# Optimization experiments

Hardware: AMD Instinct MI355X
Metric: run time of the kernel (lower is better)

The kernel has to match this reference:

```python
import jax, jax.numpy as jnp
import numpy as np

N_NODES = 50000
N_EDGES = 800000
IN_DIM = 128
IN_CH = 64
HIDDEN = 64
OUT_CH = 128
NUM_CLS = 16
NUM_GRAPHS = 512


def setup_inputs() -> dict:
    key = jax.random.key(0)
    ks = jax.random.split(key, 16)
    s = 0.02
    x = jax.random.normal(ks[0], (N_NODES, IN_DIM), jnp.float32)
    edge_index = jax.random.randint(ks[1], (2, N_EDGES), 0, N_NODES, jnp.int64)
    batch = jnp.sort(jax.random.randint(ks[2], (N_NODES,), 0, NUM_GRAPHS, jnp.int64))
    return {
        "x": x,
        "edge_index": edge_index,
        "batch": batch,
        "num_graphs": NUM_GRAPHS,
        "w_stage1": jax.random.normal(ks[3], (IN_DIM, IN_CH), jnp.float32) * s,
        "b_stage1": jnp.zeros((IN_CH,), jnp.float32),
        "rel1_w": jax.random.normal(ks[4], (IN_CH, HIDDEN), jnp.float32) * s,
        "rel1_b": jnp.zeros((HIDDEN,), jnp.float32),
        "root1_w": jax.random.normal(ks[5], (IN_CH, HIDDEN), jnp.float32) * s,
        "rel2_w": jax.random.normal(ks[6], (HIDDEN, 2 * HIDDEN), jnp.float32) * s,
        "rel2_b": jnp.zeros((2 * HIDDEN,), jnp.float32),
        "root2_w": jax.random.normal(ks[7], (HIDDEN, 2 * HIDDEN), jnp.float32) * s,
        "rel3_w": jax.random.normal(ks[8], (2 * HIDDEN, OUT_CH), jnp.float32) * s,
        "rel3_b": jnp.zeros((OUT_CH,), jnp.float32),
        "root3_w": jax.random.normal(ks[9], (2 * HIDDEN, OUT_CH), jnp.float32) * s,
        "lin_w": jax.random.normal(ks[10], (OUT_CH, NUM_CLS), jnp.float32) * s,
        "lin_b": jnp.zeros((NUM_CLS,), jnp.float32),
    }


def graph_conv(x, src, dst, rel_w, rel_b, root_w, n_nodes):
    # PyG GraphConv(aggr='add'): lin_rel(sum_{j in N(i)} x_j) + lin_root(x_i)
    agg = jax.ops.segment_sum(x[src], dst, num_segments=n_nodes)  # [N, in]
    return agg @ rel_w + rel_b + x @ root_w


def reference(x, edge_index, batch, num_graphs,
              w_stage1, b_stage1,
              rel1_w, rel1_b, root1_w,
              rel2_w, rel2_b, root2_w,
              rel3_w, rel3_b, root3_w,
              lin_w, lin_b):
    src, dst = edge_index[0], edge_index[1]
    n = x.shape[0]
    h = x @ w_stage1 + b_stage1                                   # [N, IN_CH]
    h = jax.nn.relu(graph_conv(h, src, dst, rel1_w, rel1_b, root1_w, n))
    h = jax.nn.relu(graph_conv(h, src, dst, rel2_w, rel2_b, root2_w, n))
    h = jax.nn.relu(graph_conv(h, src, dst, rel3_w, rel3_b, root3_w, n))
    # global mean pool over graphs
    sums = jax.ops.segment_sum(h, batch, num_segments=num_graphs)  # [G, OUT_CH]
    cnt = jax.ops.segment_sum(jnp.ones((n,), h.dtype), batch, num_segments=num_graphs)
    pooled = sums / jnp.maximum(cnt, 1.0)[:, None]
    # dropout treated as identity (deterministic eval reference)
    return pooled @ lin_w + lin_b                                  # [G, NUM_CLS]
```

## Files before the change

kernel.cpp:

```cpp
#include <hip/hip_runtime.h>
#include <hip/hip_bf16.h>

#define N_NODES 50000
#define N_EDGES 800000
#define IN_DIM  128
#define IN_CH   64
#define HIDDEN  64
#define OUT_CH  128
#define NUM_CLS 16
#define NUM_G   512
#define NBUK    ((N_NODES + 255) >> 8)
#define BCAP    6144
#define EPB_A   4096
#define S1BLK   782

typedef __attribute__((ext_vector_type(8))) short short8;
typedef __attribute__((ext_vector_type(4))) float f32x4;

__device__ inline float bits2f(unsigned short u) {
  unsigned x = (unsigned)u << 16;
  float f;
  __builtin_memcpy(&f, &x, 4);
  return f;
}
__device__ inline unsigned short f2bits(float v) {
  __hip_bfloat16 b = __float2bfloat16(v);
  unsigned short s;
  __builtin_memcpy(&s, &b, 2);
  return s;
}
__device__ inline short8 zero8() {
  short8 z;
#pragma unroll
  for (int i = 0; i < 8; ++i) z[i] = 0;
  return z;
}
__device__ inline void acc2(float& a0, float& a1, unsigned v) {
  a0 += bits2f((unsigned short)v);
  a1 += bits2f((unsigned short)(v >> 16));
}
__device__ inline void accu4(float* a, uint4 v) {
  acc2(a[0], a[1], v.x); acc2(a[2], a[3], v.y);
  acc2(a[4], a[5], v.z); acc2(a[6], a[7], v.w);
}

__device__ inline void stage1_wave(const float* __restrict__ Ap,
    const short* __restrict__ Wa, const float* __restrict__ bias,
    unsigned short* __restrict__ outp, int rbase, int lane) {
  constexpr int DIN = 128, DOUT = 64, KT = DIN / 32, CT = DOUT / 16;
  const int m = lane & 15;
  const int q = lane >> 4;
  const int row = rbase + m;
  const bool ok = row < N_NODES;

  short8 afr[KT];
#pragma unroll
  for (int kt = 0; kt < KT; ++kt) {
    short8 f = zero8();
    if (ok) {
      const float* ap = Ap + (size_t)row * DIN + kt * 32 + q * 8;
      float4 x0 = *(const float4*)ap;
      float4 x1 = *(const float4*)(ap + 4);
      f[0] = (short)f2bits(x0.x); f[1] = (short)f2bits(x0.y);
      f[2] = (short)f2bits(x0.z); f[3] = (short)f2bits(x0.w);
      f[4] = (short)f2bits(x1.x); f[5] = (short)f2bits(x1.y);
      f[6] = (short)f2bits(x1.z); f[7] = (short)f2bits(x1.w);
    }
    afr[kt] = f;
  }
#pragma unroll
  for (int ct = 0; ct < CT; ++ct) {
    f32x4 c = {0.f, 0.f, 0.f, 0.f};
#pragma unroll
    for (int kt = 0; kt < KT; ++kt) {
      short8 b = *(const short8*)(Wa + ((size_t)(kt * CT + ct) * 64 + lane) * 8);
      c = __builtin_amdgcn_mfma_f32_16x16x32_bf16(afr[kt], b, c, 0, 0, 0);
    }
    float bv = bias[ct * 16 + m];
#pragma unroll
    for (int r = 0; r < 4; ++r) {
      int ro = rbase + q * 4 + r;
      if (ro < N_NODES) outp[(size_t)ro * DOUT + ct * 16 + m] = f2bits(c[r] + bv);
    }
  }
}

template <int DIN, int DOUT>
__global__ __launch_bounds__(64) void k_fused(
    const unsigned short* __restrict__ h, const int* __restrict__ esrc,
    const int* __restrict__ off, const short* __restrict__ Wa,
    const short* __restrict__ Wh, const float* __restrict__ bias,
    unsigned short* __restrict__ outp) {
  constexpr int KT = DIN / 32;
  constexpr int CT = DOUT / 16;
  const int lane = threadIdx.x;
  const int m = lane & 15;
  const int q = lane >> 4;
  const int node = blockIdx.x * 16 + m;

  float acc[KT][8];
#pragma unroll
  for (int kt = 0; kt < KT; ++kt)
#pragma unroll
    for (int j = 0; j < 8; ++j) acc[kt][j] = 0.f;

  {
    int e = off[node], end = off[node + 1];
    const unsigned short* hq = h + q * 8;
    for (; e + 2 <= end; e += 2) {
      int s0 = esrc[e], s1 = esrc[e + 1];
      const unsigned short* r0 = hq + (size_t)s0 * DIN;
      const unsigned short* r1 = hq + (size_t)s1 * DIN;
#pragma unroll
      for (int kt = 0; kt < KT; ++kt) {
        uint4 va = *(const uint4*)(r0 + kt * 32);
        uint4 vb = *(const uint4*)(r1 + kt * 32);
        accu4(acc[kt], va);
        accu4(acc[kt], vb);
      }
    }
    if (e < end) {
      const unsigned short* r0 = hq + (size_t)esrc[e] * DIN;
#pragma unroll
      for (int kt = 0; kt < KT; ++kt)
        accu4(acc[kt], *(const uint4*)(r0 + kt * 32));
    }
  }

  short8 afr[KT], hfr[KT];
#pragma unroll
  for (int kt = 0; kt < KT; ++kt) {
    short8 f;
#pragma unroll
    for (int j = 0; j < 8; ++j) f[j] = (short)f2bits(acc[kt][j]);
    afr[kt] = f;
    hfr[kt] = *(const short8*)(h + (size_t)node * DIN + kt * 32 + q * 8);
  }

  const int rbase = blockIdx.x * 16;
#pragma unroll
  for (int ct = 0; ct < CT; ++ct) {
    f32x4 c = {0.f, 0.f, 0.f, 0.f};
#pragma unroll
    for (int kt = 0; kt < KT; ++kt) {
      short8 b = *(const short8*)(Wa + ((size_t)(kt * CT + ct) * 64 + lane) * 8);
      c = __builtin_amdgcn_mfma_f32_16x16x32_bf16(afr[kt], b, c, 0, 0, 0);
      short8 bh = *(const short8*)(Wh + ((size_t)(kt * CT + ct) * 64 + lane) * 8);
      c = __builtin_amdgcn_mfma_f32_16x16x32_bf16(hfr[kt], bh, c, 0, 0, 0);
    }
    float bv = bias[ct * 16 + m];
#pragma unroll
    for (int r = 0; r < 4; ++r) {
      int row = rbase + q * 4 + r;
      outp[(size_t)row * DOUT + ct * 16 + m] = f2bits(fmaxf(c[r] + bv, 0.f));
    }
  }
}

template <int DIN, int DOUT>
__device__ inline void pack1(const float* __restrict__ W, short* __restrict__ o,
                             int t) {
  constexpr int CT = DOUT / 16;
  int j = t & 7;
  int lane = (t >> 3) & 63;
  int kc = t >> 9;
  int ct = kc % CT;
  int kt = kc / CT;
  int k = kt * 32 + (lane >> 4) * 8 + j;
  int n = ct * 16 + (lane & 15);
  o[t] = (short)f2bits(W[k * DOUT + n]);
}

struct PackArgs {
  const float *w1, *r1, *o1, *r2, *o2, *r3, *o3;
  short *w1p, *r1p, *o1p, *r2p, *o2p, *r3p, *o3p;
};

__device__ inline void packflat(const PackArgs& a, int t) {
  if      (t < 8192)  pack1<128, 64>(a.w1, a.w1p, t);
  else if (t < 12288) pack1<64, 64>(a.r1, a.r1p, t - 8192);
  else if (t < 16384) pack1<64, 64>(a.o1, a.o1p, t - 12288);
  else if (t < 24576) pack1<64, 128>(a.r2, a.r2p, t - 16384);
  else if (t < 32768) pack1<64, 128>(a.o2, a.o2p, t - 24576);
  else if (t < 49152) pack1<128, 128>(a.r3, a.r3p, t - 32768);
  else if (t < 65536) pack1<128, 128>(a.o3, a.o3p, t - 49152);
}

__global__ __launch_bounds__(256) void k_bucketA(const int* __restrict__ src,
    const int* __restrict__ dst, int* __restrict__ bcnt,
    unsigned* __restrict__ bbuf, PackArgs pk) {
  __shared__ int hist[NBUK], sbase[NBUK], lcur[NBUK];
  const int t = threadIdx.x;

  {
    int g0 = blockIdx.x * 256 + t;
    packflat(pk, g0);
    packflat(pk, g0 + 50176);
  }

  for (int i = t; i < NBUK; i += 256) { hist[i] = 0; lcur[i] = 0; }
  __syncthreads();
  const int e0 = blockIdx.x * EPB_A;
  int s_[16], d_[16];
  int cnt = 0;
#pragma unroll
  for (int k = 0; k < 16; ++k) {
    int e = e0 + k * 256 + t;
    if (e < N_EDGES) {
      s_[cnt] = src[e]; d_[cnt] = dst[e];
      atomicAdd(&hist[d_[cnt] >> 8], 1);
      cnt++;
    }
  }
  __syncthreads();
  for (int i = t; i < NBUK; i += 256) sbase[i] = atomicAdd(&bcnt[i], hist[i]);
  __syncthreads();
  for (int k = 0; k < cnt; ++k) {
    int b = d_[k] >> 8;
    int pos = sbase[b] + atomicAdd(&lcur[b], 1);
    if (pos < BCAP)
      bbuf[(size_t)b * BCAP + pos] =
          ((unsigned)s_[k] << 8) | ((unsigned)d_[k] & 255u);
  }
}

__global__ __launch_bounds__(256) void k_bfin_s1(const int* __restrict__ bcnt,
    const unsigned* __restrict__ bbuf, int* __restrict__ off,
    int* __restrict__ esrc,
    const float* __restrict__ x, const short* __restrict__ w1p,
    const float* __restrict__ b1, unsigned short* __restrict__ P) {
  if (blockIdx.x >= NBUK) {
    const int bs = blockIdx.x - NBUK;
    const int wave = threadIdx.x >> 6;
    const int lane = threadIdx.x & 63;
    stage1_wave(x, w1p, b1, P, bs * 64 + wave * 16, lane);
    return;
  }

  __shared__ int cnt[256], s[256], soff[256];
  const int b = blockIdx.x;
  const int t = threadIdx.x;

  int bv0 = (t < NBUK) ? min(bcnt[t], BCAP) : 0;
  s[t] = bv0;
  __syncthreads();
  for (int st = 1; st < 256; st <<= 1) {
    int v = (t >= st) ? s[t - st] : 0;
    __syncthreads();
    s[t] += v;
    __syncthreads();
  }
  __shared__ int bbase_s;
  if (t == b) bbase_s = s[t] - bv0;
  if (b == 0 && t == NBUK - 1) off[N_NODES] = s[t];
  __syncthreads();
  const int bb = bbase_s;

  cnt[t] = 0;
  __syncthreads();
  int n = min(bcnt[b], BCAP);
  for (int i = t; i < n; i += 256)
    atomicAdd(&cnt[bbuf[(size_t)b * BCAP + i] & 255u], 1);
  __syncthreads();
  int v0 = cnt[t];
  s[t] = v0;
  __syncthreads();
  for (int st = 1; st < 256; st <<= 1) {
    int v = (t >= st) ? s[t - st] : 0;
    __syncthreads();
    s[t] += v;
    __syncthreads();
  }
  int myoff = bb + s[t] - v0;
  int node = b * 256 + t;
  if (node < N_NODES) off[node] = myoff;
  soff[t] = myoff;
  cnt[t] = 0;
  __syncthreads();
  for (int i = t; i < n; i += 256) {
    unsigned p = bbuf[(size_t)b * BCAP + i];
    int l = (int)(p & 255u);
    int r = atomicAdd(&cnt[l], 1);
    esrc[soff[l] + r] = (int)(p >> 8);
  }
}

__device__ inline int lbound(const int* __restrict__ a, int n, int v) {
  int lo = 0, hi = n;
  while (lo < hi) {
    int m = (lo + hi) >> 1;
    if (a[m] < v) lo = m + 1; else hi = m;
  }
  return lo;
}

__global__ __launch_bounds__(128) void k_poolhead(const unsigned short* __restrict__ h3,
    const int* __restrict__ batch, const float* __restrict__ lw,
    const float* __restrict__ lb, float* __restrict__ out) {
  __shared__ float sp[128];
  int g = blockIdx.x;
  int t = threadIdx.x;
  int lo = lbound(batch, N_NODES, g);
  int hi = lbound(batch, N_NODES, g + 1);
  float a0 = 0.f, a1 = 0.f, a2 = 0.f, a3 = 0.f;
  int r = lo;
  for (; r + 4 <= hi; r += 4) {
    a0 += bits2f(h3[(size_t)(r + 0) * OUT_CH + t]);
    a1 += bits2f(h3[(size_t)(r + 1) * OUT_CH + t]);
    a2 += bits2f(h3[(size_t)(r + 2) * OUT_CH + t]);
    a3 += bits2f(h3[(size_t)(r + 3) * OUT_CH + t]);
  }
  for (; r < hi; ++r) a0 += bits2f(h3[(size_t)r * OUT_CH + t]);
  float inv = (hi > lo) ? 1.f / (float)(hi - lo) : 0.f;
  sp[t] = ((a0 + a1) + (a2 + a3)) * inv;
  __syncthreads();
  if (t < NUM_CLS) {
    float s = lb[t];
#pragma unroll
    for (int k = 0; k < OUT_CH; ++k) s = fmaf(sp[k], lw[k * NUM_CLS + t], s);
    out[g * NUM_CLS + t] = s;
  }
}

extern "C" void kernel_launch(void* const* d_in, const int* in_sizes, int n_in,
                              void* d_out, int out_size, void* d_ws, size_t ws_size,
                              hipStream_t stream) {
  const float* x      = (const float*)d_in[0];
  const int*   ei     = (const int*)d_in[1];
  const int*   batch  = (const int*)d_in[2];
  const float* w1     = (const float*)d_in[4];
  const float* b1     = (const float*)d_in[5];
  const float* rel1w  = (const float*)d_in[6];
  const float* rel1b  = (const float*)d_in[7];
  const float* root1w = (const float*)d_in[8];
  const float* rel2w  = (const float*)d_in[9];
  const float* rel2b  = (const float*)d_in[10];
  const float* root2w = (const float*)d_in[11];
  const float* rel3w  = (const float*)d_in[12];
  const float* rel3b  = (const float*)d_in[13];
  const float* root3w = (const float*)d_in[14];
  const float* linw   = (const float*)d_in[15];
  const float* linb   = (const float*)d_in[16];
  const int* src = ei;
  const int* dst = ei + N_EDGES;
  float* out = (float*)d_out;

  unsigned short* P = (unsigned short*)d_ws;
  unsigned short* Q = P + (size_t)N_NODES * 128;
  unsigned short* R = Q + (size_t)N_NODES * 128;
  short* WP = (short*)(R + (size_t)N_NODES * 128);
  short* w1p  = WP;
  short* r1p  = w1p + 8192;
  short* o1p  = r1p + 4096;
  short* r2p  = o1p + 4096;
  short* o2p  = r2p + 8192;
  short* r3p  = o2p + 8192;
  short* o3p  = r3p + 16384;
  int* off     = (int*)(o3p + 16384);
  int* bcnt    = off + (N_NODES + 1);
  int* esrc    = bcnt + NBUK + 3;
  unsigned* bbuf = (unsigned*)(esrc + N_EDGES);

  PackArgs pk = {w1, rel1w, root1w, rel2w, root2w, rel3w, root3w,
                 w1p, r1p, o1p, r2p, o2p, r3p, o3p};

  hipMemsetAsync(bcnt, 0, NBUK * sizeof(int), stream);
  k_bucketA<<<(N_EDGES + EPB_A - 1) / EPB_A, 256, 0, stream>>>(src, dst, bcnt,
                                                               bbuf, pk);
  k_bfin_s1<<<NBUK + S1BLK, 256, 0, stream>>>(bcnt, bbuf, off, esrc,
                                              x, w1p, b1, P);

  const int GF = (N_NODES + 15) / 16;

  k_fused<64, 64><<<GF, 64, 0, stream>>>(P, esrc, off, r1p, o1p, rel1b, R);
  k_fused<64, 128><<<GF, 64, 0, stream>>>(R, esrc, off, r2p, o2p, rel2b, Q);
  k_fused<128, 128><<<GF, 64, 0, stream>>>(Q, esrc, off, r3p, o3p, rel3b, P);
  k_poolhead<<<NUM_G, 128, 0, stream>>>(P, batch, linw, linb, out);
}
```

Measured before the change: 240.4 us.

## Split fused GraphConv feature dimension across two waves with LDS reduction

Each 16-node block now uses two wavefronts, each gathering and accumulating half of the input feature dimension (K split). Each wave computes partial MFMA products for half the output tiles, exchanges them through shared memory, and sums them before bias and ReLU. This doubles wave-level parallelism for the edge gather, giving more memory-level parallelism and latency hiding. The cost is a block barrier, LDS traffic for the partial sums, and each wave re-reading the edge indices.

After: 244.6 us. Within noise of the previous version (+1.8%).

```diff
diff --git a/kernel.cpp b/kernel.cpp
--- a/kernel.cpp
+++ b/kernel.cpp
@@ -86,33 +86,37 @@
 }
 
 template <int DIN, int DOUT>
-__global__ __launch_bounds__(64) void k_fused(
+__global__ __launch_bounds__(128) void k_fused(
     const unsigned short* __restrict__ h, const int* __restrict__ esrc,
     const int* __restrict__ off, const short* __restrict__ Wa,
     const short* __restrict__ Wh, const float* __restrict__ bias,
     unsigned short* __restrict__ outp) {
   constexpr int KT = DIN / 32;
   constexpr int CT = DOUT / 16;
-  const int lane = threadIdx.x;
+  constexpr int KTH = KT / 2;
+  constexpr int CTH = CT / 2;
+  __shared__ float comb[CT * 4 * 64];
+  const int wid = threadIdx.x >> 6;
+  const int lane = threadIdx.x & 63;
   const int m = lane & 15;
   const int q = lane >> 4;
   const int node = blockIdx.x * 16 + m;
 
-  float acc[KT][8];
-#pragma unroll
-  for (int kt = 0; kt < KT; ++kt)
+  float acc[KTH][8];
+#pragma unroll
+  for (int kt = 0; kt < KTH; ++kt)
 #pragma unroll
     for (int j = 0; j < 8; ++j) acc[kt][j] = 0.f;
 
   {
     int e = off[node], end = off[node + 1];
-    const unsigned short* hq = h + q * 8;
+    const unsigned short* hq = h + q * 8 + wid * (KTH * 32);
     for (; e + 2 <= end; e += 2) {
       int s0 = esrc[e], s1 = esrc[e + 1];
       const unsigned short* r0 = hq + (size_t)s0 * DIN;
       const unsigned short* r1 = hq + (size_t)s1 * DIN;
 #pragma unroll
-      for (int kt = 0; kt < KT; ++kt) {
+      for (int kt = 0; kt < KTH; ++kt) {
         uint4 va = *(const uint4*)(r0 + kt * 32);
         uint4 vb = *(const uint4*)(r1 + kt * 32);
         accu4(acc[kt], va);
@@ -122,37 +126,57 @@
     if (e < end) {
       const unsigned short* r0 = hq + (size_t)esrc[e] * DIN;
 #pragma unroll
-      for (int kt = 0; kt < KT; ++kt)
+      for (int kt = 0; kt < KTH; ++kt)
         accu4(acc[kt], *(const uint4*)(r0 + kt * 32));
     }
   }
 
-  short8 afr[KT], hfr[KT];
-#pragma unroll
-  for (int kt = 0; kt < KT; ++kt) {
+  short8 afr[KTH], hfr[KTH];
+#pragma unroll
+  for (int kt = 0; kt < KTH; ++kt) {
     short8 f;
 #pragma unroll
     for (int j = 0; j < 8; ++j) f[j] = (short)f2bits(acc[kt][j]);
     afr[kt] = f;
-    hfr[kt] = *(const short8*)(h + (size_t)node * DIN + kt * 32 + q * 8);
+    hfr[kt] = *(const short8*)(h + (size_t)node * DIN +
+                               (wid * KTH + kt) * 32 + q * 8);
   }
 
   const int rbase = blockIdx.x * 16;
 #pragma unroll
-  for (int ct = 0; ct < CT; ++ct) {
+  for (int i = 0; i < CTH; ++i) {
+    const int ct = (1 - wid) * CTH + i;
     f32x4 c = {0.f, 0.f, 0.f, 0.f};
 #pragma unroll
-    for (int kt = 0; kt < KT; ++kt) {
-      short8 b = *(const short8*)(Wa + ((size_t)(kt * CT + ct) * 64 + lane) * 8);
+    for (int kt = 0; kt < KTH; ++kt) {
+      const int gkt = wid * KTH + kt;
+      short8 b = *(const short8*)(Wa + ((size_t)(gkt * CT + ct) * 64 + lane) * 8);
       c = __builtin_amdgcn_mfma_f32_16x16x32_bf16(afr[kt], b, c, 0, 0, 0);
-      short8 bh = *(const short8*)(Wh + ((size_t)(kt * CT + ct) * 64 + lane) * 8);
+      short8 bh = *(const short8*)(Wh + ((size_t)(gkt * CT + ct) * 64 + lane) * 8);
+      c = __builtin_amdgcn_mfma_f32_16x16x32_bf16(hfr[kt], bh, c, 0, 0, 0);
+    }
+#pragma unroll
+    for (int r = 0; r < 4; ++r) comb[(ct * 4 + r) * 64 + lane] = c[r];
+  }
+  __syncthreads();
+#pragma unroll
+  for (int i = 0; i < CTH; ++i) {
+    const int ct = wid * CTH + i;
+    f32x4 c = {0.f, 0.f, 0.f, 0.f};
+#pragma unroll
+    for (int kt = 0; kt < KTH; ++kt) {
+      const int gkt = wid * KTH + kt;
+      short8 b = *(const short8*)(Wa + ((size_t)(gkt * CT + ct) * 64 + lane) * 8);
+      c = __builtin_amdgcn_mfma_f32_16x16x32_bf16(afr[kt], b, c, 0, 0, 0);
+      short8 bh = *(const short8*)(Wh + ((size_t)(gkt * CT + ct) * 64 + lane) * 8);
       c = __builtin_amdgcn_mfma_f32_16x16x32_bf16(hfr[kt], bh, c, 0, 0, 0);
     }
     float bv = bias[ct * 16 + m];
 #pragma unroll
     for (int r = 0; r < 4; ++r) {
       int row = rbase + q * 4 + r;
-      outp[(size_t)row * DOUT + ct * 16 + m] = f2bits(fmaxf(c[r] + bv, 0.f));
+      float v = c[r] + comb[(ct * 4 + r) * 64 + lane] + bv;
+      outp[(size_t)row * DOUT + ct * 16 + m] = f2bits(fmaxf(v, 0.f));
     }
   }
 }
@@ -372,8 +396,8 @@
 
   const int GF = (N_NODES + 15) / 16;
 
-  k_fused<64, 64><<<GF, 64, 0, stream>>>(P, esrc, off, r1p, o1p, rel1b, R);
-  k_fused<64, 128><<<GF, 64, 0, stream>>>(R, esrc, off, r2p, o2p, rel2b, Q);
-  k_fused<128, 128><<<GF, 64, 0, stream>>>(Q, esrc, off, r3p, o3p, rel3b, P);
+  k_fused<64, 64><<<GF, 128, 0, stream>>>(P, esrc, off, r1p, o1p, rel1b, R);
+  k_fused<64, 128><<<GF, 128, 0, stream>>>(R, esrc, off, r2p, o2p, rel2b, Q);
+  k_fused<128, 128><<<GF, 128, 0, stream>>>(Q, esrc, off, r3p, o3p, rel3b, P);
   k_poolhead<<<NUM_G, 128, 0, stream>>>(P, batch, linw, linb, out);
 }
```
